# Kernel tuning notes

Hardware: AMD Instinct MI355X
Metric: run time of the kernel (lower is better)

The kernel has to match this reference:

```python
import jax, jax.numpy as jnp
import numpy as np

B, L, D, S = 4, 4096, 1024, 16
EPS = 1e-5  # nn.LayerNorm default


def setup_inputs() -> dict:
    key = jax.random.key(0)
    ks = jax.random.split(key, 8)
    s = 0.02
    return {
        "x_seq": jax.random.normal(ks[0], (B, L, D), jnp.float32),
        "h_prev": jnp.zeros((B, S), jnp.float32),
        "gamma": jnp.ones((D,), jnp.float32),
        "beta": jnp.zeros((D,), jnp.float32),
        "W_in": jax.random.normal(ks[1], (D, D), jnp.float32) * s,
        "b_in": jnp.zeros((D,), jnp.float32),
        "W_A": jax.random.normal(ks[2], (D, S), jnp.float32) * s,
        "b_A": jnp.zeros((S,), jnp.float32),
        "W_B": jax.random.normal(ks[3], (D, S), jnp.float32) * s,
        "b_B": jnp.zeros((S,), jnp.float32),
        "W_C": jax.random.normal(ks[4], (D, S), jnp.float32) * s,
        "b_C": jnp.zeros((S,), jnp.float32),
        "W_dt": jax.random.normal(ks[5], (D, 1), jnp.float32) * s,
        "b_dt": jnp.zeros((1,), jnp.float32),
        "W_out": jax.random.normal(ks[6], (D, D), jnp.float32) * s,
        "b_out": jnp.zeros((D,), jnp.float32),
    }


def _layernorm(x, gamma, beta):
    mu = jnp.mean(x, axis=-1, keepdims=True)
    var = jnp.mean(jnp.square(x - mu), axis=-1, keepdims=True)
    return (x - mu) * jax.lax.rsqrt(var + EPS) * gamma + beta


def reference(x_seq, h_prev, gamma, beta, W_in, b_in, W_A, b_A, W_B, b_B,
              W_C, b_C, W_dt, b_dt, W_out, b_out):
    # pre-scan projections (all batched over (B, L))
    x = _layernorm(x_seq, gamma, beta)
    x = jax.nn.silu(x @ W_in + b_in)                    # (B, L, D)
    log_A = -jax.nn.softplus(x @ W_A + b_A)             # (B, L, S)
    B_t = x @ W_B + b_B                                 # (B, L, S)
    C_t = x @ W_C + b_C                                 # (B, L, S)
    dt = jax.nn.softplus(x @ W_dt + b_dt)               # (B, L, 1)
    A_disc = jnp.exp(log_A * dt)                        # (B, L, S)
    u = jnp.mean(x, axis=-1, keepdims=True)             # (B, L, 1)
    Bu = (B_t * dt) * u                                 # (B, L, S)

    # selective scan: h_t = A_t * h_{t-1} + Bu_t  over time axis
    def step(h, inp):
        a_t, bu_t = inp
        h = a_t * h + bu_t
        return h, h

    h_final, hs = jax.lax.scan(
        step, h_prev,
        (jnp.swapaxes(A_disc, 0, 1), jnp.swapaxes(Bu, 0, 1)))
    hs = jnp.swapaxes(hs, 0, 1)                         # (B, L, S)

    y = jnp.sum(C_t * hs, axis=-1, keepdims=True)       # (B, L, 1)
    y_seq = (x * y) @ W_out + b_out + x_seq             # (B, L, D)
    return y_seq, h_final
```

## Files before the change

kernel.cpp:

```cpp
#include <hip/hip_runtime.h>

typedef unsigned short u16;
typedef unsigned int u32;
typedef __attribute__((ext_vector_type(8))) short short8;
typedef __attribute__((ext_vector_type(4))) float f32x4;

#define B_ 4
#define L_ 4096
#define D_ 1024
#define S_ 16
#define M_ (B_ * L_)
#define NBG 64
#define LC 64

__device__ __forceinline__ float b2f(u16 h) {
    unsigned u = ((unsigned)h) << 16;
    return __builtin_bit_cast(float, u);
}
__device__ __forceinline__ u16 f2b(float f) {
    unsigned u = __builtin_bit_cast(unsigned, f);
    u += 0x7fffu + ((u >> 16) & 1u);
    return (u16)(u >> 16);
}
__device__ __forceinline__ float softplus_f(float z) {
    return z > 20.f ? z : log1pf(__expf(z));
}
__device__ __forceinline__ void gload16(const u16* g, const u16* l) {
    __builtin_amdgcn_global_load_lds(
        (const __attribute__((address_space(1))) u32*)g,
        (__attribute__((address_space(3))) u32*)l, 16, 0, 0);
}

__global__ __launch_bounds__(256) void prep_kernel(
    const float* __restrict__ W0, u16* __restrict__ Wt0,
    const float* __restrict__ W1, u16* __restrict__ Wt1,
    const float* __restrict__ WA, const float* __restrict__ WB,
    const float* __restrict__ WC, const float* __restrict__ Wdt,
    u16* __restrict__ Wp) {
    int b = blockIdx.x, tid = threadIdx.x;
    if (b < 2048) {
        const float* W = (b >> 10) ? W1 : W0;
        u16* Wt = (b >> 10) ? Wt1 : Wt0;
        int by = (b >> 5) & 31, bx = b & 31;
        int x = tid & 31, ty = tid >> 5;
        __shared__ float t[32][33];
        for (int j = ty; j < 32; j += 8)
            t[j][x] = W[(size_t)(by * 32 + j) * D_ + bx * 32 + x];
        __syncthreads();
        for (int j = ty; j < 32; j += 8)
            Wt[(size_t)(bx * 32 + j) * D_ + by * 32 + x] = f2b(t[x][j]);
    } else {
        int idx = (b - 2048) * 256 + tid;
        int s = idx >> 10, k = idx & 1023;
        float v;
        if (s < 16)       v = WA[k * 16 + s];
        else if (s < 32)  v = WB[k * 16 + (s - 16)];
        else if (s < 48)  v = WC[k * 16 + (s - 32)];
        else if (s == 48) v = Wdt[k];
        else if (s == 49) v = 1.0f / 1024.0f;
        else              v = 0.f;
        Wp[idx] = f2b(v);
    }
}

__global__ __launch_bounds__(256) void ln_kernel(
    const float* __restrict__ x, const float* __restrict__ gamma,
    const float* __restrict__ beta, u16* __restrict__ out) {
    int row = blockIdx.x, tid = threadIdx.x;
    const float4 v = *(const float4*)&x[(size_t)row * D_ + tid * 4];
    float s = v.x + v.y + v.z + v.w;
    float q = v.x * v.x + v.y * v.y + v.z * v.z + v.w * v.w;
    for (int o = 32; o > 0; o >>= 1) { s += __shfl_down(s, o); q += __shfl_down(q, o); }
    __shared__ float ss[4], qq[4];
    int w = tid >> 6, lane = tid & 63;
    if (lane == 0) { ss[w] = s; qq[w] = q; }
    __syncthreads();
    if (tid == 0) {
        float S = ss[0] + ss[1] + ss[2] + ss[3];
        float Q = qq[0] + qq[1] + qq[2] + qq[3];
        float mu = S * (1.f / D_);
        float var = Q * (1.f / D_) - mu * mu;
        ss[0] = mu; qq[0] = rsqrtf(var + 1e-5f);
    }
    __syncthreads();
    float mu = ss[0], rs = qq[0];
    const float4 gv = *(const float4*)&gamma[tid * 4];
    const float4 bv = *(const float4*)&beta[tid * 4];
    ushort4 o4;
    o4.x = f2b((v.x - mu) * rs * gv.x + bv.x);
    o4.y = f2b((v.y - mu) * rs * gv.y + bv.y);
    o4.z = f2b((v.z - mu) * rs * gv.z + bv.z);
    o4.w = f2b((v.w - mu) * rs * gv.w + bv.w);
    *(ushort4*)&out[(size_t)row * D_ + tid * 4] = o4;
}

template <int EPI>
__global__ __launch_bounds__(512, 1) void gemm256(
    const u16* __restrict__ A, const u16* __restrict__ Bt,
    const float* __restrict__ bias, const float* __restrict__ resid,
    const float* __restrict__ yrow,
    u16* __restrict__ outB, float* __restrict__ outF,
    int M, int N, int K, int nTileN) {
    __shared__ u16 sm[65536];
    const int TILES = K >> 6;

    int nwg = gridDim.x;
    int bid = blockIdx.x;
    int swz = (bid & 7) * (nwg >> 3) + (bid >> 3);
    int bx = swz % nTileN, by = swz / nTileN;
    int rowBase = by * 256, colBase = bx * 256;

    int tid = threadIdx.x;
    int lane = tid & 63, w = tid >> 6;
    int wr = w >> 2, wc = w & 3;
    int lr = lane & 15, lg = lane >> 4;
    const unsigned woff = (unsigned)((lr * 32 + lg * 8) ^ ((lr & 8) ? 16 : 0));

    int sub = w;
    int pos = sub >> 1;
    int kblk = sub & 1;
    int r = lane >> 2;
    int chunk = (lane & 3) ^ ((r & 8) ? 2 : 0);
    int rowoff = (pos & 1) * 16 + (pos >> 1) * 128;
    const u16* gAs = A  + (size_t)(rowBase + rowoff + r) * K + kblk * 32 + chunk * 8;
    const u16* gBs = Bt + (size_t)(colBase + rowoff + r) * K + kblk * 32 + chunk * 8;
    const unsigned subb = (unsigned)sub * 512u;

#define STAGEPAIR(tau, p)                                                        \
    do {                                                                         \
        unsigned _bb = (unsigned)((tau) & 1) * 32768u;                           \
        size_t _go = (size_t)(p) * 32 * K + (size_t)(tau) * 64;                  \
        gload16(gBs + _go, &sm[_bb + 16384u + (unsigned)(p) * 4096u + subb]);    \
        gload16(gAs + _go, &sm[_bb + (unsigned)(p) * 4096u + subb]);             \
    } while (0)

    f32x4 acc[8][4] = {};

    STAGEPAIR(0, 0); STAGEPAIR(0, 1); STAGEPAIR(0, 2); STAGEPAIR(0, 3);
    if (TILES > 1) { STAGEPAIR(1, 0); STAGEPAIR(1, 1); STAGEPAIR(1, 2); }
    asm volatile("s_waitcnt vmcnt(6)" ::: "memory");
    __builtin_amdgcn_s_barrier();

    for (int t = 0; t < TILES; ++t) {
        const unsigned bb = (unsigned)(t & 1) * 32768u;
        short8 bfr[4][2], afr[2][2];
        if (t + 1 < TILES) STAGEPAIR(t + 1, 3);
#pragma unroll
        for (int n = 0; n < 4; n++) {
            int rb = wc * 4 + n;
            unsigned bo = bb + 16384u + (unsigned)(((rb & 7) >> 1)) * 4096u
                        + (unsigned)(((rb & 1) + ((rb >> 3) << 1)) << 1) * 512u + woff;
            bfr[n][0] = *(const short8*)&sm[bo];
            bfr[n][1] = *(const short8*)&sm[bo + 512u];
        }
#pragma unroll
        for (int dm = 0; dm < 2; dm++) {
            unsigned ao = bb + (unsigned)((dm + (wr << 1)) << 1) * 512u + woff;
            afr[dm][0] = *(const short8*)&sm[ao];
            afr[dm][1] = *(const short8*)&sm[ao + 512u];
        }
        __builtin_amdgcn_s_barrier();
        __builtin_amdgcn_s_setprio(1);
#pragma unroll
        for (int dm = 0; dm < 2; dm++)
#pragma unroll
            for (int n = 0; n < 4; n++)
#pragma unroll
                for (int ks = 0; ks < 2; ks++)
                    acc[dm][n] = __builtin_amdgcn_mfma_f32_16x16x32_bf16(
                        afr[dm][ks], bfr[n][ks], acc[dm][n], 0, 0, 0);
        __builtin_amdgcn_s_setprio(0);
        __builtin_amdgcn_s_barrier();
#pragma unroll
        for (int q = 1; q < 4; q++) {
            if (t + 2 < TILES) STAGEPAIR(t + 2, q - 1);
#pragma unroll
            for (int dm = 0; dm < 2; dm++) {
                int m = q * 2 + dm;
                unsigned ao = bb + (unsigned)q * 4096u
                            + (unsigned)(((m & 1) + (wr << 1)) << 1) * 512u + woff;
                afr[dm][0] = *(const short8*)&sm[ao];
                afr[dm][1] = *(const short8*)&sm[ao + 512u];
            }
            __builtin_amdgcn_s_barrier();
            __builtin_amdgcn_s_setprio(1);
#pragma unroll
            for (int dm = 0; dm < 2; dm++)
#pragma unroll
                for (int n = 0; n < 4; n++)
#pragma unroll
                    for (int ks = 0; ks < 2; ks++)
                        acc[q * 2 + dm][n] = __builtin_amdgcn_mfma_f32_16x16x32_bf16(
                            afr[dm][ks], bfr[n][ks], acc[q * 2 + dm][n], 0, 0, 0);
            __builtin_amdgcn_s_setprio(0);
            if (q == 3) {
                if (t + 2 < TILES)      asm volatile("s_waitcnt vmcnt(6)" ::: "memory");
                else if (t + 1 < TILES) asm volatile("s_waitcnt vmcnt(0)" ::: "memory");
            }
            __builtin_amdgcn_s_barrier();
        }
    }
#undef STAGEPAIR

    if (EPI == 1) {
        float bcol[4];
#pragma unroll
        for (int n = 0; n < 4; n++) bcol[n] = bias[colBase + wc * 64 + n * 16 + lr];
#pragma unroll
        for (int m = 0; m < 8; m++)
#pragma unroll
            for (int n = 0; n < 4; n++)
#pragma unroll
                for (int j = 0; j < 4; j++) {
                    int row = wr * 128 + m * 16 + lg * 4 + j;
                    int col = wc * 64 + n * 16 + lr;
                    float v = acc[m][n][j] + bcol[n];
                    v = v / (1.f + __expf(-v));
                    int cbs = (col >> 4) ^ lg;
                    sm[row * 256 + cbs * 16 + (col & 15)] = f2b(v);
                }
        __syncthreads();
        int rr = tid >> 1, half = tid & 1;
        u16* gout = outB + (size_t)(rowBase + rr) * N + colBase;
#pragma unroll
        for (int q = 0; q < 8; q++) {
            int cb = half * 8 + q;
            int cbs = cb ^ ((rr >> 2) & 3);
            *(uint4*)&gout[cb * 16] = *(const uint4*)&sm[rr * 256 + cbs * 16];
        }
    } else {
        float bcol[4];
#pragma unroll
        for (int n = 0; n < 4; n++) bcol[n] = bias[colBase + wc * 64 + n * 16 + lr];
#pragma unroll
        for (int m = 0; m < 8; m++) {
            float yr[4];
#pragma unroll
            for (int j = 0; j < 4; j++)
                yr[j] = yrow[rowBase + wr * 128 + m * 16 + lg * 4 + j];
#pragma unroll
            for (int n = 0; n < 4; n++)
#pragma unroll
                for (int j = 0; j < 4; j++) {
                    int row = rowBase + wr * 128 + m * 16 + lg * 4 + j;
                    int col = colBase + wc * 64 + n * 16 + lr;
                    size_t o = (size_t)row * N + col;
                    outF[o] = acc[m][n][j] * yr[j] + bcol[n] + resid[o];
                }
        }
    }
}

__global__ __launch_bounds__(256) void proj_kernel(
    const u16* __restrict__ X, const u16* __restrict__ Wp,
    const float* __restrict__ bA, const float* __restrict__ bB,
    const float* __restrict__ bC, const float* __restrict__ bdt,
    float* __restrict__ Ad, float* __restrict__ Bu, float* __restrict__ Ct) {
    __shared__ u16 Xs[2][64][32];
    __shared__ u16 Ws[2][64][32];
    int rowBase = blockIdx.x * 64;
    int tid = threadIdx.x, lane = tid & 63, w = tid >> 6;
    int lr = lane & 15, lg = lane >> 4;
    f32x4 acc[4] = {};
    const int sr = lane >> 2, sc = (lane & 3) * 8;
    const u16* gX = &X[(size_t)(rowBase + w * 16 + sr) * 1024 + sc];
    const u16* gW = &Wp[(size_t)(w * 16 + sr) * 1024 + sc];

#define PSTAGE(d, k0)                              \
    do {                                           \
        gload16(gX + (k0), &Xs[d][w * 16][0]);     \
        gload16(gW + (k0), &Ws[d][w * 16][0]);     \
    } while (0)

    PSTAGE(0, 0);
    __syncthreads();
    int cur = 0;
    for (int k0 = 0; k0 < 1024; k0 += 32) {
        if (k0 + 32 < 1024) PSTAGE(cur ^ 1, k0 + 32);
        short8 a = *(const short8*)&Xs[cur][w * 16 + lr][lg * 8];
#pragma unroll
        for (int n = 0; n < 4; n++) {
            short8 b = *(const short8*)&Ws[cur][n * 16 + lr][lg * 8];
            acc[n] = __builtin_amdgcn_mfma_f32_16x16x32_bf16(a, b, acc[n], 0, 0, 0);
        }
        __syncthreads();
        cur ^= 1;
    }
#undef PSTAGE
    float bdt0 = bdt[0];
#pragma unroll
    for (int j = 0; j < 4; j++) {
        int row = rowBase + w * 16 + lg * 4 + j;
        float dtr = __shfl(acc[3][j], lg * 16 + 0, 64);
        float uv  = __shfl(acc[3][j], lg * 16 + 1, 64);
        float dt = softplus_f(dtr + bdt0);
        float zA = acc[0][j] + bA[lr];
        float zB = acc[1][j] + bB[lr];
        float zC = acc[2][j] + bC[lr];
        size_t o = (size_t)row * 16 + lr;
        Ad[o] = __expf(-dt * softplus_f(zA));
        Bu[o] = zB * dt * uv;
        Ct[o] = zC;
    }
}

__global__ __launch_bounds__(1024) void scan_part1(
    const float* __restrict__ Ad, const float* __restrict__ Bu,
    float* __restrict__ Pb, float* __restrict__ Qb) {
    int b = blockIdx.x >> 6, g = blockIdx.x & 63;
    int tid = threadIdx.x;
    int s = tid & 15, c = tid >> 4;
    size_t idx = ((size_t)b * L_ + g * LC + c) * S_ + s;
    float a = Ad[idx], bu = Bu[idx];
    __shared__ float Ps[16][64], Qs[16][64];
    Ps[s][c] = a; Qs[s][c] = bu;
    __syncthreads();
    if (tid < 16) {
        float P = 1.f, Q = 0.f;
        for (int cc = 0; cc < 64; cc++) {
            float pa = Ps[tid][cc], qa = Qs[tid][cc];
            P = pa * P;
            Q = pa * Q + qa;
        }
        int o = (b * NBG + g) * S_ + tid;
        Pb[o] = P; Qb[o] = Q;
    }
}

__global__ __launch_bounds__(64) void scan_part2(
    const float* __restrict__ Pb, const float* __restrict__ Qb,
    const float* __restrict__ hprev, float* __restrict__ Hb,
    float* __restrict__ hfinal) {
    int t = threadIdx.x;
    int b = t >> 4, s = t & 15;
    float h = hprev[b * S_ + s];
    for (int g = 0; g < NBG; g++) {
        int o = (b * NBG + g) * S_ + s;
        Hb[o] = h;
        h = Pb[o] * h + Qb[o];
    }
    hfinal[b * S_ + s] = h;
}

__global__ __launch_bounds__(1024) void scan_part3(
    const float* __restrict__ Ad, const float* __restrict__ Bu,
    const float* __restrict__ Ct, const float* __restrict__ Hb,
    float* __restrict__ y) {
    int b = blockIdx.x >> 6, g = blockIdx.x & 63;
    int tid = threadIdx.x;
    int s = tid & 15, c = tid >> 4;
    size_t idx = ((size_t)b * L_ + g * LC + c) * S_ + s;
    float a = Ad[idx], bu = Bu[idx];
    __shared__ float Ps[16][64], Qs[16][64], Hin[16][65];
    Ps[s][c] = a; Qs[s][c] = bu;
    __syncthreads();
    if (tid < 16) {
        float h = Hb[(b * NBG + g) * S_ + tid];
        for (int cc = 0; cc < 64; cc++) {
            Hin[tid][cc] = h;
            h = Ps[tid][cc] * h + Qs[tid][cc];
        }
    }
    __syncthreads();
    float h = a * Hin[s][c] + bu;
    float p = Ct[idx] * h;
    p += __shfl_xor(p, 1);
    p += __shfl_xor(p, 2);
    p += __shfl_xor(p, 4);
    p += __shfl_xor(p, 8);
    if (s == 0) y[(size_t)b * L_ + g * LC + c] = p;
}

extern "C" void kernel_launch(void* const* d_in, const int* in_sizes, int n_in,
                              void* d_out, int out_size, void* d_ws, size_t ws_size,
                              hipStream_t stream) {
    const float* x_seq  = (const float*)d_in[0];
    const float* h_prev = (const float*)d_in[1];
    const float* gamma  = (const float*)d_in[2];
    const float* beta   = (const float*)d_in[3];
    const float* W_in   = (const float*)d_in[4];
    const float* b_in   = (const float*)d_in[5];
    const float* W_A    = (const float*)d_in[6];
    const float* b_A    = (const float*)d_in[7];
    const float* W_B    = (const float*)d_in[8];
    const float* b_B    = (const float*)d_in[9];
    const float* W_C    = (const float*)d_in[10];
    const float* b_C    = (const float*)d_in[11];
    const float* W_dt   = (const float*)d_in[12];
    const float* b_dt   = (const float*)d_in[13];
    const float* W_out  = (const float*)d_in[14];
    const float* b_out  = (const float*)d_in[15];

    char* ws = (char*)d_ws;
    u16*   x_ln   = (u16*)(ws + 0);
    u16*   x      = (u16*)(ws + 33554432);
    u16*   Wt_in  = (u16*)(ws + 67108864);
    u16*   Wt_out = (u16*)(ws + 69206016);
    u16*   Wp     = (u16*)(ws + 71303168);
    float* Ad     = (float*)(ws + 71434240);
    float* Bu     = (float*)(ws + 72482816);
    float* Ct     = (float*)(ws + 73531392);
    float* yv     = (float*)(ws + 74579968);
    float* Pb     = (float*)(ws + 74645504);
    float* Qb     = (float*)(ws + 74661888);
    float* Hb     = (float*)(ws + 74678272);
    float* out    = (float*)d_out;

    prep_kernel<<<2304, 256, 0, stream>>>(W_in, Wt_in, W_out, Wt_out,
                                          W_A, W_B, W_C, W_dt, Wp);
    ln_kernel<<<M_, 256, 0, stream>>>(x_seq, gamma, beta, x_ln);
    gemm256<1><<<(M_ / 256) * (D_ / 256), 512, 0, stream>>>(
        x_ln, Wt_in, b_in, nullptr, nullptr, x, nullptr, M_, D_, D_, D_ / 256);
    proj_kernel<<<M_ / 64, 256, 0, stream>>>(x, Wp, b_A, b_B, b_C, b_dt, Ad, Bu, Ct);
    scan_part1<<<B_ * NBG, 1024, 0, stream>>>(Ad, Bu, Pb, Qb);
    scan_part2<<<1, 64, 0, stream>>>(Pb, Qb, h_prev, Hb, out + (size_t)M_ * D_);
    scan_part3<<<B_ * NBG, 1024, 0, stream>>>(Ad, Bu, Ct, Hb, yv);
    gemm256<2><<<(M_ / 256) * (D_ / 256), 512, 0, stream>>>(
        x, Wt_out, b_out, x_seq, yv, nullptr, out, M_, D_, D_, D_ / 256);
}
```

Before: 153.3 us.

## Simplify GEMM main loop to per-tile double buffering and fold scan_part2 into part3

The GEMM K-loop drops the fine-grained staged prefetch with five barriers per tile. It now issues the whole next tile's global loads at the top of each iteration, double-buffers A fragments in registers, and syncs once per tile with vmcnt(0). Separately, scan_part2 is removed: each scan_part3 block recomputes its own chunk-carry state serially from Pb/Qb, and the last chunk writes h_final. This saves one kernel launch, at the cost of redundant serial work and reduced overlap in the GEMM.

```diff
diff --git a/kernel.cpp b/kernel.cpp
--- a/kernel.cpp
+++ b/kernel.cpp
@@ -126,79 +126,66 @@
     const u16* gBs = Bt + (size_t)(colBase + rowoff + r) * K + kblk * 32 + chunk * 8;
     const unsigned subb = (unsigned)sub * 512u;
 
-#define STAGEPAIR(tau, p)                                                        \
+#define STAGEPAIR(sbb, tau, p)                                                   \
     do {                                                                         \
-        unsigned _bb = (unsigned)((tau) & 1) * 32768u;                           \
         size_t _go = (size_t)(p) * 32 * K + (size_t)(tau) * 64;                  \
-        gload16(gBs + _go, &sm[_bb + 16384u + (unsigned)(p) * 4096u + subb]);    \
-        gload16(gAs + _go, &sm[_bb + (unsigned)(p) * 4096u + subb]);             \
+        gload16(gBs + _go, &sm[(sbb) + 16384u + (unsigned)(p) * 4096u + subb]);  \
+        gload16(gAs + _go, &sm[(sbb) + (unsigned)(p) * 4096u + subb]);           \
     } while (0)
 
     f32x4 acc[8][4] = {};
 
-    STAGEPAIR(0, 0); STAGEPAIR(0, 1); STAGEPAIR(0, 2); STAGEPAIR(0, 3);
-    if (TILES > 1) { STAGEPAIR(1, 0); STAGEPAIR(1, 1); STAGEPAIR(1, 2); }
-    asm volatile("s_waitcnt vmcnt(6)" ::: "memory");
+    STAGEPAIR(0u, 0, 0); STAGEPAIR(0u, 0, 1); STAGEPAIR(0u, 0, 2); STAGEPAIR(0u, 0, 3);
+    asm volatile("s_waitcnt vmcnt(0)" ::: "memory");
     __builtin_amdgcn_s_barrier();
 
     for (int t = 0; t < TILES; ++t) {
         const unsigned bb = (unsigned)(t & 1) * 32768u;
-        short8 bfr[4][2], afr[2][2];
-        if (t + 1 < TILES) STAGEPAIR(t + 1, 3);
+        const unsigned sbnext = (unsigned)((t + 1) & 1) * 32768u;
+        if (t + 1 < TILES) {
+            STAGEPAIR(sbnext, t + 1, 0); STAGEPAIR(sbnext, t + 1, 1);
+            STAGEPAIR(sbnext, t + 1, 2); STAGEPAIR(sbnext, t + 1, 3);
+        }
+        short8 bfr[4][2], afr[2][2][2];
 #pragma unroll
         for (int n = 0; n < 4; n++) {
             int rb = wc * 4 + n;
-            unsigned bo = bb + 16384u + (unsigned)(((rb & 7) >> 1)) * 4096u
-                        + (unsigned)(((rb & 1) + ((rb >> 3) << 1)) << 1) * 512u + woff;
+            unsigned bo = bb + 16384u + (unsigned)((rb & 7) >> 1) * 4096u
+                        + (unsigned)((rb & 1) + ((rb >> 3) << 1)) * 1024u + woff;
             bfr[n][0] = *(const short8*)&sm[bo];
             bfr[n][1] = *(const short8*)&sm[bo + 512u];
         }
 #pragma unroll
-        for (int dm = 0; dm < 2; dm++) {
-            unsigned ao = bb + (unsigned)((dm + (wr << 1)) << 1) * 512u + woff;
-            afr[dm][0] = *(const short8*)&sm[ao];
-            afr[dm][1] = *(const short8*)&sm[ao + 512u];
-        }
+        for (int dm = 0; dm < 2; dm++)
+#pragma unroll
+            for (int ks = 0; ks < 2; ks++)
+                afr[0][dm][ks] = *(const short8*)&sm[bb + (unsigned)(dm + 2 * wr) * 1024u
+                                                    + (unsigned)ks * 512u + woff];
+#pragma unroll
+        for (int q = 0; q < 4; q++) {
+            if (q < 3) {
+#pragma unroll
+                for (int dm = 0; dm < 2; dm++)
+#pragma unroll
+                    for (int ks = 0; ks < 2; ks++)
+                        afr[(q + 1) & 1][dm][ks] =
+                            *(const short8*)&sm[bb + (unsigned)(q + 1) * 4096u
+                                                + (unsigned)(dm + 2 * wr) * 1024u
+                                                + (unsigned)ks * 512u + woff];
+            }
+            __builtin_amdgcn_s_setprio(1);
+#pragma unroll
+            for (int ks = 0; ks < 2; ks++)
+#pragma unroll
+                for (int dm = 0; dm < 2; dm++)
+#pragma unroll
+                    for (int n = 0; n < 4; n++)
+                        acc[q * 2 + dm][n] = __builtin_amdgcn_mfma_f32_16x16x32_bf16(
+                            afr[q & 1][dm][ks], bfr[n][ks], acc[q * 2 + dm][n], 0, 0, 0);
+            __builtin_amdgcn_s_setprio(0);
+        }
+        if (t + 1 < TILES) asm volatile("s_waitcnt vmcnt(0)" ::: "memory");
         __builtin_amdgcn_s_barrier();
-        __builtin_amdgcn_s_setprio(1);
-#pragma unroll
-        for (int dm = 0; dm < 2; dm++)
-#pragma unroll
-            for (int n = 0; n < 4; n++)
-#pragma unroll
-                for (int ks = 0; ks < 2; ks++)
-                    acc[dm][n] = __builtin_amdgcn_mfma_f32_16x16x32_bf16(
-                        afr[dm][ks], bfr[n][ks], acc[dm][n], 0, 0, 0);
-        __builtin_amdgcn_s_setprio(0);
-        __builtin_amdgcn_s_barrier();
-#pragma unroll
-        for (int q = 1; q < 4; q++) {
-            if (t + 2 < TILES) STAGEPAIR(t + 2, q - 1);
-#pragma unroll
-            for (int dm = 0; dm < 2; dm++) {
-                int m = q * 2 + dm;
-                unsigned ao = bb + (unsigned)q * 4096u
-                            + (unsigned)(((m & 1) + (wr << 1)) << 1) * 512u + woff;
-                afr[dm][0] = *(const short8*)&sm[ao];
-                afr[dm][1] = *(const short8*)&sm[ao + 512u];
-            }
-            __builtin_amdgcn_s_barrier();
-            __builtin_amdgcn_s_setprio(1);
-#pragma unroll
-            for (int dm = 0; dm < 2; dm++)
-#pragma unroll
-                for (int n = 0; n < 4; n++)
-#pragma unroll
-                    for (int ks = 0; ks < 2; ks++)
-                        acc[q * 2 + dm][n] = __builtin_amdgcn_mfma_f32_16x16x32_bf16(
-                            afr[dm][ks], bfr[n][ks], acc[q * 2 + dm][n], 0, 0, 0);
-            __builtin_amdgcn_s_setprio(0);
-            if (q == 3) {
-                if (t + 2 < TILES)      asm volatile("s_waitcnt vmcnt(6)" ::: "memory");
-                else if (t + 1 < TILES) asm volatile("s_waitcnt vmcnt(0)" ::: "memory");
-            }
-            __builtin_amdgcn_s_barrier();
-        }
     }
 #undef STAGEPAIR
 
@@ -327,25 +314,11 @@
     }
 }
 
-__global__ __launch_bounds__(64) void scan_part2(
-    const float* __restrict__ Pb, const float* __restrict__ Qb,
-    const float* __restrict__ hprev, float* __restrict__ Hb,
-    float* __restrict__ hfinal) {
-    int t = threadIdx.x;
-    int b = t >> 4, s = t & 15;
-    float h = hprev[b * S_ + s];
-    for (int g = 0; g < NBG; g++) {
-        int o = (b * NBG + g) * S_ + s;
-        Hb[o] = h;
-        h = Pb[o] * h + Qb[o];
-    }
-    hfinal[b * S_ + s] = h;
-}
-
 __global__ __launch_bounds__(1024) void scan_part3(
     const float* __restrict__ Ad, const float* __restrict__ Bu,
-    const float* __restrict__ Ct, const float* __restrict__ Hb,
-    float* __restrict__ y) {
+    const float* __restrict__ Ct, const float* __restrict__ Pb,
+    const float* __restrict__ Qb, const float* __restrict__ hprev,
+    float* __restrict__ y, float* __restrict__ hfinal) {
     int b = blockIdx.x >> 6, g = blockIdx.x & 63;
     int tid = threadIdx.x;
     int s = tid & 15, c = tid >> 4;
@@ -355,11 +328,16 @@
     Ps[s][c] = a; Qs[s][c] = bu;
     __syncthreads();
     if (tid < 16) {
-        float h = Hb[(b * NBG + g) * S_ + tid];
+        float h = hprev[b * S_ + tid];
+        for (int gg = 0; gg < g; gg++) {
+            int o = (b * NBG + gg) * S_ + tid;
+            h = Pb[o] * h + Qb[o];
+        }
         for (int cc = 0; cc < 64; cc++) {
             Hin[tid][cc] = h;
             h = Ps[tid][cc] * h + Qs[tid][cc];
         }
+        if (g == NBG - 1) hfinal[b * S_ + tid] = h;
     }
     __syncthreads();
     float h = a * Hin[s][c] + bu;
@@ -403,7 +381,6 @@
     float* yv     = (float*)(ws + 74579968);
     float* Pb     = (float*)(ws + 74645504);
     float* Qb     = (float*)(ws + 74661888);
-    float* Hb     = (float*)(ws + 74678272);
     float* out    = (float*)d_out;
 
     prep_kernel<<<2304, 256, 0, stream>>>(W_in, Wt_in, W_out, Wt_out,
@@ -413,8 +390,8 @@
         x_ln, Wt_in, b_in, nullptr, nullptr, x, nullptr, M_, D_, D_, D_ / 256);
     proj_kernel<<<M_ / 64, 256, 0, stream>>>(x, Wp, b_A, b_B, b_C, b_dt, Ad, Bu, Ct);
     scan_part1<<<B_ * NBG, 1024, 0, stream>>>(Ad, Bu, Pb, Qb);
-    scan_part2<<<1, 64, 0, stream>>>(Pb, Qb, h_prev, Hb, out + (size_t)M_ * D_);
-    scan_part3<<<B_ * NBG, 1024, 0, stream>>>(Ad, Bu, Ct, Hb, yv);
+    scan_part3<<<B_ * NBG, 1024, 0, stream>>>(Ad, Bu, Ct, Pb, Qb, h_prev,
+                                              yv, out + (size_t)M_ * D_);
     gemm256<2><<<(M_ / 256) * (D_ / 256), 512, 0, stream>>>(
         x, Wt_out, b_out, x_seq, yv, nullptr, out, M_, D_, D_, D_ / 256);
 }
```

New measurement: 155.5 us. Within noise of the previous version (+1.4%).
